# Optimization experiments

Measured on AMD Instinct MI355X. Metric: run time of the kernel, lower is better.

Reference implementation:

```python
import jax, jax.numpy as jnp
import numpy as np

HEADS = 8
EPS = 1e-5


def setup_inputs() -> dict:
    key = jax.random.key(0)
    ks = jax.random.split(key, 8)
    B, S, D = 4, 2048, 512
    inputs = jax.random.normal(ks[0], (B, S, D), dtype=jnp.float32)
    mask = jnp.ones((B, S), dtype=jnp.int32)
    sc = 1.0 / np.sqrt(D)
    # torch Linear weights stored transposed as [in, out] for x @ W
    W_qkv = jax.random.uniform(ks[1], (D, 3 * D), jnp.float32, -sc, sc)
    b_qkv = jax.random.uniform(ks[2], (3 * D,), jnp.float32, -sc, sc)
    W_o = jax.random.uniform(ks[3], (D, D), jnp.float32, -sc, sc)
    b_o = jax.random.uniform(ks[4], (D,), jnp.float32, -sc, sc)
    gamma = jnp.ones((D,), jnp.float32)
    beta = jnp.zeros((D,), jnp.float32)
    return {"inputs": inputs, "mask": mask, "W_qkv": W_qkv, "b_qkv": b_qkv,
            "W_o": W_o, "b_o": b_o, "gamma": gamma, "beta": beta}


def reference(inputs, mask, W_qkv, b_qkv, W_o, b_o, gamma, beta):
    B, S, D = inputs.shape
    H = HEADS
    dh = D // H
    t = inputs @ W_qkv + b_qkv                      # [B,S,3D]
    q, k, v = jnp.split(t, 3, axis=-1)
    # [B,S,D] -> [B,H,S,dh]
    q = q.reshape(B, S, H, dh).transpose(0, 2, 1, 3)
    k = k.reshape(B, S, H, dh).transpose(0, 2, 1, 3)
    v = v.reshape(B, S, H, dh).transpose(0, 2, 1, 3)
    # unscaled dot-product attention (is_scaled=False in the source)
    scores = jnp.einsum('bhqd,bhkd->bhqk', q, k)    # [B,H,S,S]
    key_mask = (mask > 0)[:, None, None, :]         # broadcast over heads & query rows
    scores = jnp.where(key_mask, scores, -jnp.inf)
    attn = jax.nn.softmax(scores, axis=-1)
    att = jnp.einsum('bhqk,bhkd->bhqd', attn, v)    # [B,H,S,dh]
    att = att.transpose(0, 2, 1, 3).reshape(B, S, D)
    out = att @ W_o + b_o
    x = out + att                                    # residual
    mu = jnp.mean(x, axis=-1, keepdims=True)
    var = jnp.mean(jnp.square(x - mu), axis=-1, keepdims=True)
    return (x - mu) / jnp.sqrt(var + EPS) * gamma + beta
```

## Files before the change

kernel.cpp:

```cpp
#include <hip/hip_runtime.h>
#include <cstdint>

#define S_LEN 2048
#define D_MODEL 512
#define H_NUM 8
#define DH 64
#define LOG2E 1.4426950408889634f

typedef __attribute__((ext_vector_type(8))) short bf16x8;
typedef __attribute__((ext_vector_type(8))) unsigned short u16x8;
typedef __attribute__((ext_vector_type(4))) float f32x4;

__device__ inline unsigned short f2bf(float x) {
    unsigned int u = __builtin_bit_cast(unsigned int, x);
    u += 0x7fffu + ((u >> 16) & 1u);
    return (unsigned short)(u >> 16);
}
__device__ inline float bf2f(unsigned short u) {
    return __builtin_bit_cast(float, (unsigned int)u << 16);
}

__device__ inline void async_ld16(const unsigned short* g, unsigned short* l) {
    __builtin_amdgcn_global_load_lds(
        (const __attribute__((address_space(1))) unsigned int*)(const unsigned int*)g,
        (__attribute__((address_space(3))) unsigned int*)(unsigned int*)l,
        16, 0, 0);
}

__global__ __launch_bounds__(256) void prep(
    const float* __restrict__ X, const float* __restrict__ Wqkv,
    const float* __restrict__ Wo,
    unsigned short* __restrict__ Xb, unsigned short* __restrict__ WqkvT,
    unsigned short* __restrict__ WoT)
{
    __shared__ float tile[32][36];
    const int blk = blockIdx.x;
    const int tid = threadIdx.x;
    if (blk < 1024) {
        const int base = blk * 4096 + tid * 16;
        #pragma unroll
        for (int i = 0; i < 4; ++i) {
            float4 v = *(const float4*)(X + base + i * 4);
            ushort4 o;
            o.x = f2bf(v.x); o.y = f2bf(v.y); o.z = f2bf(v.z); o.w = f2bf(v.w);
            *(ushort4*)(Xb + base + i * 4) = o;
        }
        return;
    }
    const float* src; unsigned short* dst; int N, t;
    if (blk < 1792) { src = Wqkv; dst = WqkvT; N = 1536; t = blk - 1024; }
    else            { src = Wo;   dst = WoT;   N = 512;  t = blk - 1792; }
    const int tnx = N / 32;
    const int bx = t % tnx;
    const int by = t / tnx;
    const int row = tid >> 3;
    const int c4  = (tid & 7) * 4;
    *(float4*)&tile[row][c4] = *(const float4*)(src + (size_t)(by * 32 + row) * N + bx * 32 + c4);
    __syncthreads();
    ushort4 o;
    o.x = f2bf(tile[c4 + 0][row]);
    o.y = f2bf(tile[c4 + 1][row]);
    o.z = f2bf(tile[c4 + 2][row]);
    o.w = f2bf(tile[c4 + 3][row]);
    *(ushort4*)(dst + (size_t)(bx * 32 + row) * 512 + by * 32 + c4) = o;
}

__global__ __launch_bounds__(256) void qkv_mfma(
    const unsigned short* __restrict__ Xb, const unsigned short* __restrict__ WT,
    const float* __restrict__ bias,
    unsigned short* __restrict__ Q, unsigned short* __restrict__ K,
    unsigned short* __restrict__ Vt)
{
    __shared__ unsigned short sA[128 * 64];
    __shared__ unsigned short sB[128 * 64];
    const int tid  = threadIdx.x;
    const int w    = tid >> 6;
    const int lane = tid & 63;
    const int l16  = lane & 15;
    const int quad = lane >> 4;
    const int wm = w >> 1, wn = w & 1;
    const int n0 = blockIdx.x * 128;
    const int m0 = blockIdx.y * 128;

    const unsigned short* gA[4]; const unsigned short* gB[4];
    unsigned short *lA[4], *lB[4];
    #pragma unroll
    for (int j = 0; j < 4; ++j) {
        const int ci = tid + j * 256;
        const int row = ci >> 3;
        const int col = ((ci & 7) ^ (row & 7)) * 8;
        gA[j] = Xb + (size_t)(m0 + row) * 512 + col;
        gB[j] = WT + (size_t)(n0 + row) * 512 + col;
        lA[j] = sA + ci * 8 - lane * 8;
        lB[j] = sB + ci * 8 - lane * 8;
    }

    f32x4 acc[4][4] = {};
    for (int k0 = 0; k0 < 512; k0 += 64) {
        __syncthreads();
        #pragma unroll
        for (int j = 0; j < 4; ++j) {
            async_ld16(gA[j] + k0, lA[j]);
            async_ld16(gB[j] + k0, lB[j]);
        }
        __syncthreads();
        bf16x8 a[4][2], bfr[4][2];
        #pragma unroll
        for (int mi = 0; mi < 4; ++mi) {
            const int row = wm * 64 + mi * 16 + l16;
            a[mi][0] = *(const bf16x8*)&sA[row * 64 + ((quad       ^ (row & 7)) * 8)];
            a[mi][1] = *(const bf16x8*)&sA[row * 64 + (((4 + quad) ^ (row & 7)) * 8)];
        }
        #pragma unroll
        for (int ni = 0; ni < 4; ++ni) {
            const int row = wn * 64 + ni * 16 + l16;
            bfr[ni][0] = *(const bf16x8*)&sB[row * 64 + ((quad       ^ (row & 7)) * 8)];
            bfr[ni][1] = *(const bf16x8*)&sB[row * 64 + (((4 + quad) ^ (row & 7)) * 8)];
        }
        #pragma unroll
        for (int mi = 0; mi < 4; ++mi)
            #pragma unroll
            for (int ni = 0; ni < 4; ++ni) {
                acc[mi][ni] = __builtin_amdgcn_mfma_f32_16x16x32_bf16(a[mi][0], bfr[ni][0], acc[mi][ni], 0, 0, 0);
                acc[mi][ni] = __builtin_amdgcn_mfma_f32_16x16x32_bf16(a[mi][1], bfr[ni][1], acc[mi][ni], 0, 0, 0);
            }
    }

    const int which = n0 >> 9;
    const int h = ((n0 & 511) >> 6) + wn;
    const int b = m0 >> 11;
    const int sbase = (m0 & 2047) + wm * 64;
    float bv[4];
    #pragma unroll
    for (int ni = 0; ni < 4; ++ni) bv[ni] = bias[n0 + wn * 64 + ni * 16 + l16];
    if (which == 2) {
        #pragma unroll
        for (int ni = 0; ni < 4; ++ni) {
            const int dh = ni * 16 + l16;
            unsigned short* vp = Vt + ((size_t)(b * H_NUM + h) * DH + dh) * S_LEN;
            #pragma unroll
            for (int mi = 0; mi < 4; ++mi) {
                const int s0 = sbase + mi * 16 + quad * 4;
                ushort4 o;
                o.x = f2bf(acc[mi][ni][0] + bv[ni]);
                o.y = f2bf(acc[mi][ni][1] + bv[ni]);
                o.z = f2bf(acc[mi][ni][2] + bv[ni]);
                o.w = f2bf(acc[mi][ni][3] + bv[ni]);
                *(ushort4*)(vp + s0) = o;
            }
        }
    } else {
        const float qs = (which == 0) ? LOG2E : 1.0f;
        unsigned short* dst = (which == 0) ? Q : K;
        dst += (size_t)(b * H_NUM + h) * S_LEN * DH;
        #pragma unroll
        for (int mi = 0; mi < 4; ++mi)
            #pragma unroll
            for (int r = 0; r < 4; ++r) {
                const int s = sbase + mi * 16 + quad * 4 + r;
                #pragma unroll
                for (int ni = 0; ni < 4; ++ni)
                    dst[(size_t)s * DH + ni * 16 + l16] = f2bf((acc[mi][ni][r] + bv[ni]) * qs);
            }
    }
}

__global__ __launch_bounds__(256) void attn_mfma(
    const unsigned short* __restrict__ Q, const unsigned short* __restrict__ K,
    const unsigned short* __restrict__ Vt, const int* __restrict__ mask,
    unsigned short* __restrict__ att)
{
    __shared__ unsigned short sQ[64][72];
    __shared__ unsigned short sK[64 * 64];
    __shared__ unsigned short sVt[64 * 64];
    __shared__ unsigned short sP[4][16][72];
    __shared__ int smask[64];

    const int tid  = threadIdx.x;
    const int w    = tid >> 6;
    const int lane = tid & 63;
    const int l16  = lane & 15;
    const int quad = lane >> 4;
    const int qt = blockIdx.x;
    const int bh = blockIdx.y;
    const int b  = bh >> 3;
    const int h  = bh & 7;
    const size_t kbase = (size_t)bh * S_LEN * DH;
    const size_t vbase = (size_t)bh * DH * S_LEN;

    {
        const int row = tid >> 2;
        const int c16 = (tid & 3) * 16;
        const unsigned short* gq = Q + kbase + (size_t)(qt * 64 + row) * DH + c16;
        *(u16x8*)&sQ[row][c16]     = *(const u16x8*)gq;
        *(u16x8*)&sQ[row][c16 + 8] = *(const u16x8*)(gq + 8);
    }
    __syncthreads();
    const bf16x8 qf0 = *(const bf16x8*)&sQ[w * 16 + l16][quad * 8];
    const bf16x8 qf1 = *(const bf16x8*)&sQ[w * 16 + l16][32 + quad * 8];

    const int ci0 = w * 128 + lane;
    const int ci1 = ci0 + 64;
    const int r0_ = ci0 >> 3, c0_ = ((ci0 & 7) ^ (r0_ & 7)) * 8;
    const int r1_ = ci1 >> 3, c1_ = ((ci1 & 7) ^ (r1_ & 7)) * 8;
    const int kOff0 = r0_ * 64 + c0_;
    const int kOff1 = r1_ * 64 + c1_;
    const int vOff0 = r0_ * S_LEN + c0_;
    const int vOff1 = r1_ * S_LEN + c1_;
    const int lds0 = ci0 * 8 - lane * 8;
    const int lds1 = ci1 * 8 - lane * 8;

    f32x4 O[4] = {{0,0,0,0},{0,0,0,0},{0,0,0,0},{0,0,0,0}};
    float lreg[4] = {0.f, 0.f, 0.f, 0.f};
    const int psw = (quad ^ (l16 >> 2)) * 8;
    const int ksw = l16 & 7;

    for (int kt = 0; kt < 32; ++kt) {
        __syncthreads();
        {
            const unsigned short* gK = K  + kbase + (size_t)kt * 64 * DH;
            const unsigned short* gV = Vt + vbase + kt * 64;
            async_ld16(gK + kOff0, sK + lds0);
            async_ld16(gK + kOff1, sK + lds1);
            async_ld16(gV + vOff0, sVt + lds0);
            async_ld16(gV + vOff1, sVt + lds1);
            if (tid < 64) smask[tid] = mask[b * S_LEN + kt * 64 + tid];
        }
        __syncthreads();

        f32x4 c[4] = {{0,0,0,0},{0,0,0,0},{0,0,0,0},{0,0,0,0}};
        #pragma unroll
        for (int nb = 0; nb < 4; ++nb) {
            const int row = nb * 16 + l16;
            const bf16x8 kb0 = *(const bf16x8*)&sK[row * 64 + ((quad ^ ksw) * 8)];
            const bf16x8 kb1 = *(const bf16x8*)&sK[row * 64 + (((4 + quad) ^ ksw) * 8)];
            c[nb] = __builtin_amdgcn_mfma_f32_16x16x32_bf16(qf0, kb0, c[nb], 0, 0, 0);
            c[nb] = __builtin_amdgcn_mfma_f32_16x16x32_bf16(qf1, kb1, c[nb], 0, 0, 0);
        }

        float mb[4];
        #pragma unroll
        for (int nb = 0; nb < 4; ++nb)
            mb[nb] = smask[nb * 16 + l16] ? 0.f : -1e30f;
        #pragma unroll
        for (int r = 0; r < 4; ++r) {
            #pragma unroll
            for (int nb = 0; nb < 4; ++nb) {
                const float p = __builtin_amdgcn_exp2f(c[nb][r] + mb[nb]);
                lreg[r] += p;
                sP[w][quad * 4 + r][(nb * 16 + l16) ^ (quad * 8)] = f2bf(p);
            }
        }

        const bf16x8 pa0 = *(const bf16x8*)&sP[w][l16][psw];
        const bf16x8 pa1 = *(const bf16x8*)&sP[w][l16][32 + psw];
        #pragma unroll
        for (int db = 0; db < 4; ++db) {
            const int row = db * 16 + l16;
            const bf16x8 vb0 = *(const bf16x8*)&sVt[row * 64 + ((quad ^ ksw) * 8)];
            const bf16x8 vb1 = *(const bf16x8*)&sVt[row * 64 + (((4 + quad) ^ ksw) * 8)];
            O[db] = __builtin_amdgcn_mfma_f32_16x16x32_bf16(pa0, vb0, O[db], 0, 0, 0);
            O[db] = __builtin_amdgcn_mfma_f32_16x16x32_bf16(pa1, vb1, O[db], 0, 0, 0);
        }
    }

    #pragma unroll
    for (int off = 1; off < 16; off <<= 1)
        #pragma unroll
        for (int r = 0; r < 4; ++r)
            lreg[r] += __shfl_xor(lreg[r], off, 64);
    float inv[4];
    #pragma unroll
    for (int r = 0; r < 4; ++r) inv[r] = 1.0f / lreg[r];
    const size_t row0 = (size_t)b * S_LEN + qt * 64 + w * 16 + quad * 4;
    #pragma unroll
    for (int r = 0; r < 4; ++r) {
        unsigned short* op = att + (row0 + r) * D_MODEL + h * DH + l16;
        op[0]  = f2bf(O[0][r] * inv[r]);
        op[16] = f2bf(O[1][r] * inv[r]);
        op[32] = f2bf(O[2][r] * inv[r]);
        op[48] = f2bf(O[3][r] * inv[r]);
    }
}

__global__ __launch_bounds__(256) void proj_mfma(
    const unsigned short* __restrict__ attb, const unsigned short* __restrict__ WoT,
    const float* __restrict__ bo, float* __restrict__ xbuf)
{
    __shared__ unsigned short sA[128 * 32];
    __shared__ unsigned short sB[64 * 32];
    const int tid  = threadIdx.x;
    const int w    = tid >> 6;
    const int lane = tid & 63;
    const int l16  = lane & 15;
    const int quad = lane >> 4;
    const int wm = w >> 1, wn = w & 1;
    const int n0 = blockIdx.x * 64;
    const int m0 = blockIdx.y * 128;

    const int ci0 = tid, ci1 = tid + 256;
    const int rA0 = ci0 >> 2, cl0 = (((ci0 & 3) ^ (rA0 & 3)) * 8);
    const int rA1 = ci1 >> 2, cl1 = (((ci1 & 3) ^ (rA1 & 3)) * 8);
    const unsigned short* gA0 = attb + (size_t)(m0 + rA0) * 512 + cl0;
    const unsigned short* gA1 = attb + (size_t)(m0 + rA1) * 512 + cl1;
    const unsigned short* gB0 = WoT  + (size_t)(n0 + rA0) * 512 + cl0;
    unsigned short* ldsA0 = sA + ci0 * 8 - lane * 8;
    unsigned short* ldsA1 = sA + ci1 * 8 - lane * 8;
    unsigned short* ldsB0 = sB + ci0 * 8 - lane * 8;

    const int sw = (quad ^ (l16 & 3)) * 8;
    f32x4 acc[4][2] = {};

    for (int k0 = 0; k0 < 512; k0 += 32) {
        __syncthreads();
        async_ld16(gA0 + k0, ldsA0);
        async_ld16(gA1 + k0, ldsA1);
        async_ld16(gB0 + k0, ldsB0);
        __syncthreads();
        bf16x8 a[4], bfr[2];
        #pragma unroll
        for (int mi = 0; mi < 4; ++mi)
            a[mi] = *(const bf16x8*)&sA[(wm * 64 + mi * 16 + l16) * 32 + sw];
        #pragma unroll
        for (int ni = 0; ni < 2; ++ni)
            bfr[ni] = *(const bf16x8*)&sB[(wn * 32 + ni * 16 + l16) * 32 + sw];
        #pragma unroll
        for (int mi = 0; mi < 4; ++mi)
            #pragma unroll
            for (int ni = 0; ni < 2; ++ni)
                acc[mi][ni] = __builtin_amdgcn_mfma_f32_16x16x32_bf16(a[mi], bfr[ni], acc[mi][ni], 0, 0, 0);
    }

    #pragma unroll
    for (int ni = 0; ni < 2; ++ni) {
        const int n = n0 + wn * 32 + ni * 16 + l16;
        const float bv = bo[n];
        #pragma unroll
        for (int mi = 0; mi < 4; ++mi) {
            #pragma unroll
            for (int r = 0; r < 4; ++r) {
                const int m = m0 + wm * 64 + mi * 16 + quad * 4 + r;
                const float resid = bf2f(attb[(size_t)m * 512 + n]);
                xbuf[(size_t)m * 512 + n] = acc[mi][ni][r] + bv + resid;
            }
        }
    }
}

__global__ __launch_bounds__(256) void ln_kernel(
    const float* __restrict__ xbuf, const float* __restrict__ gamma,
    const float* __restrict__ beta, float* __restrict__ out)
{
    const int tid = threadIdx.x;
    const int w = tid >> 6, lane = tid & 63;
    const size_t row = (size_t)blockIdx.x * 4 + w;
    const float* xp = xbuf + row * 512 + lane * 8;
    float4 v0 = *(const float4*)xp;
    float4 v1 = *(const float4*)(xp + 4);
    float s  = v0.x + v0.y + v0.z + v0.w + v1.x + v1.y + v1.z + v1.w;
    float sq = v0.x*v0.x + v0.y*v0.y + v0.z*v0.z + v0.w*v0.w
             + v1.x*v1.x + v1.y*v1.y + v1.z*v1.z + v1.w*v1.w;
    #pragma unroll
    for (int off = 1; off < 64; off <<= 1) {
        s  += __shfl_xor(s, off, 64);
        sq += __shfl_xor(sq, off, 64);
    }
    const float mu = s * (1.0f / 512.0f);
    const float var = sq * (1.0f / 512.0f) - mu * mu;
    const float rs = rsqrtf(var + 1e-5f);
    float4 g0 = *(const float4*)(gamma + lane * 8);
    float4 g1 = *(const float4*)(gamma + lane * 8 + 4);
    float4 b0 = *(const float4*)(beta + lane * 8);
    float4 b1 = *(const float4*)(beta + lane * 8 + 4);
    float4 o0, o1;
    o0.x = (v0.x - mu) * rs * g0.x + b0.x;
    o0.y = (v0.y - mu) * rs * g0.y + b0.y;
    o0.z = (v0.z - mu) * rs * g0.z + b0.z;
    o0.w = (v0.w - mu) * rs * g0.w + b0.w;
    o1.x = (v1.x - mu) * rs * g1.x + b1.x;
    o1.y = (v1.y - mu) * rs * g1.y + b1.y;
    o1.z = (v1.z - mu) * rs * g1.z + b1.z;
    o1.w = (v1.w - mu) * rs * g1.w + b1.w;
    float* op = out + row * 512 + lane * 8;
    *(float4*)op = o0;
    *(float4*)(op + 4) = o1;
}

extern "C" void kernel_launch(void* const* d_in, const int* in_sizes, int n_in,
                              void* d_out, int out_size, void* d_ws, size_t ws_size,
                              hipStream_t stream)
{
    (void)in_sizes; (void)n_in; (void)out_size; (void)ws_size;
    const float* X    = (const float*)d_in[0];
    const int*   mask = (const int*)d_in[1];
    const float* Wqkv = (const float*)d_in[2];
    const float* bqkv = (const float*)d_in[3];
    const float* Wo   = (const float*)d_in[4];
    const float* bo   = (const float*)d_in[5];
    const float* gamma= (const float*)d_in[6];
    const float* beta = (const float*)d_in[7];
    float* out = (float*)d_out;

    const size_t NE = (size_t)4 * S_LEN * D_MODEL;
    unsigned short* ws16 = (unsigned short*)d_ws;
    unsigned short* Xb     = ws16;
    unsigned short* WqkvT  = Xb + NE;
    unsigned short* WoT    = WqkvT + 786432;
    unsigned short* Q      = WoT + 262144;
    unsigned short* K      = Q + NE;
    unsigned short* Vt     = K + NE;
    unsigned short* attb   = Vt + NE;
    float* xbuf = (float*)(attb + NE);

    prep<<<dim3(2048), 256, 0, stream>>>(X, Wqkv, Wo, Xb, WqkvT, WoT);
    qkv_mfma<<<dim3(12, 64), 256, 0, stream>>>(Xb, WqkvT, bqkv, Q, K, Vt);
    attn_mfma<<<dim3(32, 32), 256, 0, stream>>>(Q, K, Vt, mask, attb);
    proj_mfma<<<dim3(8, 64), 256, 0, stream>>>(attb, WoT, bo, xbuf);
    ln_kernel<<<dim3(2048), 256, 0, stream>>>(xbuf, gamma, beta, out);
}
```

Measured before the change: 196.9 us.

## Process 128 queries per attention block and deepen projection K-tile to 64

The attention kernel now handles two 64-row query tiles per block and reuses each K/V tile loaded into LDS for both. It computes S^T by swapping the MFMA operands, so P can be written as packed 4-wide stores and the mask can be read as a float4. Q fragments are loaded straight from global memory into registers, which removes the sQ staging buffer and one barrier. The output projection GEMM now uses a 64-wide K step with an XOR swizzle, which halves the number of barrier pairs. In exchange, the attention grid is halved to 512 blocks and each thread holds more registers, which may lower occupancy.

```diff
diff --git a/kernel.cpp b/kernel.cpp
--- a/kernel.cpp
+++ b/kernel.cpp
@@ -170,11 +170,10 @@
     const unsigned short* __restrict__ Vt, const int* __restrict__ mask,
     unsigned short* __restrict__ att)
 {
-    __shared__ unsigned short sQ[64][72];
     __shared__ unsigned short sK[64 * 64];
     __shared__ unsigned short sVt[64 * 64];
-    __shared__ unsigned short sP[4][16][72];
-    __shared__ int smask[64];
+    __shared__ unsigned short sP[4][32][72];
+    __shared__ float smbt[64];
 
     const int tid  = threadIdx.x;
     const int w    = tid >> 6;
@@ -188,16 +187,14 @@
     const size_t kbase = (size_t)bh * S_LEN * DH;
     const size_t vbase = (size_t)bh * DH * S_LEN;
 
+    bf16x8 qf[2][2];
     {
-        const int row = tid >> 2;
-        const int c16 = (tid & 3) * 16;
-        const unsigned short* gq = Q + kbase + (size_t)(qt * 64 + row) * DH + c16;
-        *(u16x8*)&sQ[row][c16]     = *(const u16x8*)gq;
-        *(u16x8*)&sQ[row][c16 + 8] = *(const u16x8*)(gq + 8);
-    }
-    __syncthreads();
-    const bf16x8 qf0 = *(const bf16x8*)&sQ[w * 16 + l16][quad * 8];
-    const bf16x8 qf1 = *(const bf16x8*)&sQ[w * 16 + l16][32 + quad * 8];
+        const unsigned short* qp = Q + kbase + (size_t)(qt * 128 + w * 16 + l16) * DH + quad * 8;
+        qf[0][0] = *(const bf16x8*)qp;
+        qf[0][1] = *(const bf16x8*)(qp + 32);
+        qf[1][0] = *(const bf16x8*)(qp + 64 * DH);
+        qf[1][1] = *(const bf16x8*)(qp + 64 * DH + 32);
+    }
 
     const int ci0 = w * 128 + lane;
     const int ci1 = ci0 + 64;
@@ -210,10 +207,8 @@
     const int lds0 = ci0 * 8 - lane * 8;
     const int lds1 = ci1 * 8 - lane * 8;
 
-    f32x4 O[4] = {{0,0,0,0},{0,0,0,0},{0,0,0,0},{0,0,0,0}};
-    float lreg[4] = {0.f, 0.f, 0.f, 0.f};
-    const int psw = (quad ^ (l16 >> 2)) * 8;
-    const int ksw = l16 & 7;
+    f32x4 O[2][4] = {};
+    float lacc[2] = {0.f, 0.f};
 
     for (int kt = 0; kt < 32; ++kt) {
         __syncthreads();
@@ -224,62 +219,81 @@
             async_ld16(gK + kOff1, sK + lds1);
             async_ld16(gV + vOff0, sVt + lds0);
             async_ld16(gV + vOff1, sVt + lds1);
-            if (tid < 64) smask[tid] = mask[b * S_LEN + kt * 64 + tid];
-        }
-        __syncthreads();
-
-        f32x4 c[4] = {{0,0,0,0},{0,0,0,0},{0,0,0,0},{0,0,0,0}};
+            if (tid < 64) smbt[tid] = mask[b * S_LEN + kt * 64 + tid] ? 0.f : -1e30f;
+        }
+        __syncthreads();
+
+        bf16x8 kb[4][2];
         #pragma unroll
         for (int nb = 0; nb < 4; ++nb) {
             const int row = nb * 16 + l16;
-            const bf16x8 kb0 = *(const bf16x8*)&sK[row * 64 + ((quad ^ ksw) * 8)];
-            const bf16x8 kb1 = *(const bf16x8*)&sK[row * 64 + (((4 + quad) ^ ksw) * 8)];
-            c[nb] = __builtin_amdgcn_mfma_f32_16x16x32_bf16(qf0, kb0, c[nb], 0, 0, 0);
-            c[nb] = __builtin_amdgcn_mfma_f32_16x16x32_bf16(qf1, kb1, c[nb], 0, 0, 0);
-        }
-
-        float mb[4];
+            const int x = row & 7;
+            kb[nb][0] = *(const bf16x8*)&sK[row * 64 + ((quad       ^ x) * 8)];
+            kb[nb][1] = *(const bf16x8*)&sK[row * 64 + (((4 + quad) ^ x) * 8)];
+        }
+        float4 mb[4];
         #pragma unroll
         for (int nb = 0; nb < 4; ++nb)
-            mb[nb] = smask[nb * 16 + l16] ? 0.f : -1e30f;
-        #pragma unroll
-        for (int r = 0; r < 4; ++r) {
+            mb[nb] = *(const float4*)&smbt[nb * 16 + quad * 4];
+
+        #pragma unroll
+        for (int t = 0; t < 2; ++t) {
+            f32x4 c[4] = {{0,0,0,0},{0,0,0,0},{0,0,0,0},{0,0,0,0}};
             #pragma unroll
             for (int nb = 0; nb < 4; ++nb) {
-                const float p = __builtin_amdgcn_exp2f(c[nb][r] + mb[nb]);
-                lreg[r] += p;
-                sP[w][quad * 4 + r][(nb * 16 + l16) ^ (quad * 8)] = f2bf(p);
-            }
-        }
-
-        const bf16x8 pa0 = *(const bf16x8*)&sP[w][l16][psw];
-        const bf16x8 pa1 = *(const bf16x8*)&sP[w][l16][32 + psw];
+                c[nb] = __builtin_amdgcn_mfma_f32_16x16x32_bf16(kb[nb][0], qf[t][0], c[nb], 0, 0, 0);
+                c[nb] = __builtin_amdgcn_mfma_f32_16x16x32_bf16(kb[nb][1], qf[t][1], c[nb], 0, 0, 0);
+            }
+            float ls = 0.f;
+            #pragma unroll
+            for (int nb = 0; nb < 4; ++nb) {
+                const float p0 = __builtin_amdgcn_exp2f(c[nb][0] + mb[nb].x);
+                const float p1 = __builtin_amdgcn_exp2f(c[nb][1] + mb[nb].y);
+                const float p2 = __builtin_amdgcn_exp2f(c[nb][2] + mb[nb].z);
+                const float p3 = __builtin_amdgcn_exp2f(c[nb][3] + mb[nb].w);
+                ls += (p0 + p1) + (p2 + p3);
+                ushort4 pk;
+                pk.x = f2bf(p0); pk.y = f2bf(p1); pk.z = f2bf(p2); pk.w = f2bf(p3);
+                *(ushort4*)&sP[w][t * 16 + l16][nb * 16 + quad * 4] = pk;
+            }
+            lacc[t] += ls;
+        }
+
+        bf16x8 vb[4][2];
         #pragma unroll
         for (int db = 0; db < 4; ++db) {
             const int row = db * 16 + l16;
-            const bf16x8 vb0 = *(const bf16x8*)&sVt[row * 64 + ((quad ^ ksw) * 8)];
-            const bf16x8 vb1 = *(const bf16x8*)&sVt[row * 64 + (((4 + quad) ^ ksw) * 8)];
-            O[db] = __builtin_amdgcn_mfma_f32_16x16x32_bf16(pa0, vb0, O[db], 0, 0, 0);
-            O[db] = __builtin_amdgcn_mfma_f32_16x16x32_bf16(pa1, vb1, O[db], 0, 0, 0);
-        }
-    }
-
-    #pragma unroll
-    for (int off = 1; off < 16; off <<= 1)
-        #pragma unroll
-        for (int r = 0; r < 4; ++r)
-            lreg[r] += __shfl_xor(lreg[r], off, 64);
-    float inv[4];
-    #pragma unroll
-    for (int r = 0; r < 4; ++r) inv[r] = 1.0f / lreg[r];
-    const size_t row0 = (size_t)b * S_LEN + qt * 64 + w * 16 + quad * 4;
-    #pragma unroll
-    for (int r = 0; r < 4; ++r) {
-        unsigned short* op = att + (row0 + r) * D_MODEL + h * DH + l16;
-        op[0]  = f2bf(O[0][r] * inv[r]);
-        op[16] = f2bf(O[1][r] * inv[r]);
-        op[32] = f2bf(O[2][r] * inv[r]);
-        op[48] = f2bf(O[3][r] * inv[r]);
+            const int x = row & 7;
+            vb[db][0] = *(const bf16x8*)&sVt[row * 64 + ((quad       ^ x) * 8)];
+            vb[db][1] = *(const bf16x8*)&sVt[row * 64 + (((4 + quad) ^ x) * 8)];
+        }
+        #pragma unroll
+        for (int t = 0; t < 2; ++t) {
+            const bf16x8 pa0 = *(const bf16x8*)&sP[w][t * 16 + l16][quad * 8];
+            const bf16x8 pa1 = *(const bf16x8*)&sP[w][t * 16 + l16][quad * 8 + 32];
+            #pragma unroll
+            for (int db = 0; db < 4; ++db) {
+                O[t][db] = __builtin_amdgcn_mfma_f32_16x16x32_bf16(pa0, vb[db][0], O[t][db], 0, 0, 0);
+                O[t][db] = __builtin_amdgcn_mfma_f32_16x16x32_bf16(pa1, vb[db][1], O[t][db], 0, 0, 0);
+            }
+        }
+    }
+
+    #pragma unroll
+    for (int t = 0; t < 2; ++t) {
+        float l = lacc[t];
+        l += __shfl_xor(l, 16, 64);
+        l += __shfl_xor(l, 32, 64);
+        #pragma unroll
+        for (int r = 0; r < 4; ++r) {
+            const float invr = 1.0f / __shfl(l, quad * 4 + r, 16);
+            const size_t grow = (size_t)b * S_LEN + qt * 128 + t * 64 + w * 16 + quad * 4 + r;
+            unsigned short* op = att + grow * D_MODEL + h * DH + l16;
+            op[0]  = f2bf(O[t][0][r] * invr);
+            op[16] = f2bf(O[t][1][r] * invr);
+            op[32] = f2bf(O[t][2][r] * invr);
+            op[48] = f2bf(O[t][3][r] * invr);
+        }
     }
 }
 
@@ -287,8 +301,8 @@
     const unsigned short* __restrict__ attb, const unsigned short* __restrict__ WoT,
     const float* __restrict__ bo, float* __restrict__ xbuf)
 {
-    __shared__ unsigned short sA[128 * 32];
-    __shared__ unsigned short sB[64 * 32];
+    __shared__ unsigned short sA[128 * 64];
+    __shared__ unsigned short sB[64 * 64];
     const int tid  = threadIdx.x;
     const int w    = tid >> 6;
     const int lane = tid & 63;
@@ -298,37 +312,53 @@
     const int n0 = blockIdx.x * 64;
     const int m0 = blockIdx.y * 128;
 
-    const int ci0 = tid, ci1 = tid + 256;
-    const int rA0 = ci0 >> 2, cl0 = (((ci0 & 3) ^ (rA0 & 3)) * 8);
-    const int rA1 = ci1 >> 2, cl1 = (((ci1 & 3) ^ (rA1 & 3)) * 8);
-    const unsigned short* gA0 = attb + (size_t)(m0 + rA0) * 512 + cl0;
-    const unsigned short* gA1 = attb + (size_t)(m0 + rA1) * 512 + cl1;
-    const unsigned short* gB0 = WoT  + (size_t)(n0 + rA0) * 512 + cl0;
-    unsigned short* ldsA0 = sA + ci0 * 8 - lane * 8;
-    unsigned short* ldsA1 = sA + ci1 * 8 - lane * 8;
-    unsigned short* ldsB0 = sB + ci0 * 8 - lane * 8;
-
-    const int sw = (quad ^ (l16 & 3)) * 8;
+    const unsigned short* gA[4]; unsigned short* lA[4];
+    const unsigned short* gB[2]; unsigned short* lB[2];
+    #pragma unroll
+    for (int j = 0; j < 4; ++j) {
+        const int ci = tid + j * 256;
+        const int row = ci >> 3;
+        const int col = ((ci & 7) ^ (row & 7)) * 8;
+        gA[j] = attb + (size_t)(m0 + row) * 512 + col;
+        lA[j] = sA + ci * 8 - lane * 8;
+    }
+    #pragma unroll
+    for (int j = 0; j < 2; ++j) {
+        const int ci = tid + j * 256;
+        const int row = ci >> 3;
+        const int col = ((ci & 7) ^ (row & 7)) * 8;
+        gB[j] = WoT + (size_t)(n0 + row) * 512 + col;
+        lB[j] = sB + ci * 8 - lane * 8;
+    }
+
     f32x4 acc[4][2] = {};
-
-    for (int k0 = 0; k0 < 512; k0 += 32) {
-        __syncthreads();
-        async_ld16(gA0 + k0, ldsA0);
-        async_ld16(gA1 + k0, ldsA1);
-        async_ld16(gB0 + k0, ldsB0);
-        __syncthreads();
-        bf16x8 a[4], bfr[2];
+    for (int k0 = 0; k0 < 512; k0 += 64) {
+        __syncthreads();
+        #pragma unroll
+        for (int j = 0; j < 4; ++j) async_ld16(gA[j] + k0, lA[j]);
+        #pragma unroll
+        for (int j = 0; j < 2; ++j) async_ld16(gB[j] + k0, lB[j]);
+        __syncthreads();
+        bf16x8 a[4][2], bfr[2][2];
+        #pragma unroll
+        for (int mi = 0; mi < 4; ++mi) {
+            const int row = wm * 64 + mi * 16 + l16;
+            a[mi][0] = *(const bf16x8*)&sA[row * 64 + ((quad       ^ (row & 7)) * 8)];
+            a[mi][1] = *(const bf16x8*)&sA[row * 64 + (((4 + quad) ^ (row & 7)) * 8)];
+        }
+        #pragma unroll
+        for (int ni = 0; ni < 2; ++ni) {
+            const int row = wn * 32 + ni * 16 + l16;
+            bfr[ni][0] = *(const bf16x8*)&sB[row * 64 + ((quad       ^ (row & 7)) * 8)];
+            bfr[ni][1] = *(const bf16x8*)&sB[row * 64 + (((4 + quad) ^ (row & 7)) * 8)];
+        }
         #pragma unroll
         for (int mi = 0; mi < 4; ++mi)
-            a[mi] = *(const bf16x8*)&sA[(wm * 64 + mi * 16 + l16) * 32 + sw];
-        #pragma unroll
-        for (int ni = 0; ni < 2; ++ni)
-            bfr[ni] = *(const bf16x8*)&sB[(wn * 32 + ni * 16 + l16) * 32 + sw];
-        #pragma unroll
-        for (int mi = 0; mi < 4; ++mi)
-            #pragma unroll
-            for (int ni = 0; ni < 2; ++ni)
-                acc[mi][ni] = __builtin_amdgcn_mfma_f32_16x16x32_bf16(a[mi], bfr[ni], acc[mi][ni], 0, 0, 0);
+            #pragma unroll
+            for (int ni = 0; ni < 2; ++ni) {
+                acc[mi][ni] = __builtin_amdgcn_mfma_f32_16x16x32_bf16(a[mi][0], bfr[ni][0], acc[mi][ni], 0, 0, 0);
+                acc[mi][ni] = __builtin_amdgcn_mfma_f32_16x16x32_bf16(a[mi][1], bfr[ni][1], acc[mi][ni], 0, 0, 0);
+            }
     }
 
     #pragma unroll
@@ -414,7 +444,7 @@
 
     prep<<<dim3(2048), 256, 0, stream>>>(X, Wqkv, Wo, Xb, WqkvT, WoT);
     qkv_mfma<<<dim3(12, 64), 256, 0, stream>>>(Xb, WqkvT, bqkv, Q, K, Vt);
-    attn_mfma<<<dim3(32, 32), 256, 0, stream>>>(Q, K, Vt, mask, attb);
+    attn_mfma<<<dim3(16, 32), 256, 0, stream>>>(Q, K, Vt, mask, attb);
     proj_mfma<<<dim3(8, 64), 256, 0, stream>>>(attb, WoT, bo, xbuf);
     ln_kernel<<<dim3(2048), 256, 0, stream>>>(xbuf, gamma, beta, out);
 }
```

Result: faster. 185.5 us (-5.8%).
